# Kernel tuning notes

Measured on AMD Instinct MI355X. Metric: run time of the kernel, lower is better.

Reference implementation:

```python
import jax, jax.numpy as jnp
import numpy as np

L2_REG = 0.25

def setup_inputs() -> dict:
    key = jax.random.key(0)
    k0, k1, k2, k3 = jax.random.split(key, 4)
    B, D, A, K = 16384, 128, 8192, 64
    image_embed = jax.random.normal(k0, (B, D), dtype=jnp.float32)
    anc_ind = jax.random.randint(k1, (A,), 0, B, dtype=jnp.int64)
    pos_ind = jax.random.randint(k2, (A,), 0, B, dtype=jnp.int64)
    neg_ind = jax.random.randint(k3, (A, K), 0, B, dtype=jnp.int64)
    return {"image_embed": image_embed, "anc_ind": anc_ind,
            "pos_ind": pos_ind, "neg_ind": neg_ind}

def reference(image_embed, anc_ind, pos_ind, neg_ind):
    # Gather anchor/positive/negative embeddings
    a = image_embed[anc_ind]          # [A, D]
    p = image_embed[pos_ind]          # [A, D]
    n = image_embed[neg_ind]          # [A, K, D]
    # inner[i, k] = a_i . (n_ik - p_i)
    inner = jnp.einsum('ad,akd->ak', a, n - p[:, None, :])  # [A, K]
    # log(1 + sum_k exp(inner)) computed stably via logaddexp(0, logsumexp)
    per_anchor = jnp.logaddexp(jnp.float32(0.0), jax.nn.logsumexp(inner, axis=1))
    npair = jnp.mean(per_anchor)
    # l2 term: mean L2 norm of all batch embeddings, added once per anchor / len -> once
    l2 = L2_REG * jnp.mean(jnp.linalg.norm(image_embed, axis=1))
    return npair + l2
```

## Files before the change

### kernel.cpp

```cpp
#include <hip/hip_runtime.h>
#include <math.h>

#define B_SZ 16384
#define D_DIM 128
#define A_SZ 8192
#define K_SZ 64
#define L2_REG_F 0.25f
#define NBLK 2048

__device__ __forceinline__ float wave_reduce_sum(float v) {
    #pragma unroll
    for (int off = 32; off > 0; off >>= 1)
        v += __shfl_xor(v, off, 64);
    return v;
}

__device__ __forceinline__ float wave_reduce_max(float v) {
    #pragma unroll
    for (int off = 32; off > 0; off >>= 1)
        v = fmaxf(v, __shfl_xor(v, off, 64));
    return v;
}

__device__ __forceinline__ float dot4(float4 a, float4 b) {
    return a.x * b.x + a.y * b.y + a.z * b.z + a.w * b.w;
}

__global__ __launch_bounds__(256) void fused_kernel(const float* __restrict__ embed,
                                                    const int* __restrict__ anc_ind,
                                                    const int* __restrict__ pos_ind,
                                                    const int* __restrict__ neg_ind,
                                                    float* __restrict__ partial) {
    __shared__ float red[4];
    const int wave = threadIdx.x >> 6;
    const int lane = threadIdx.x & 63;
    const int i    = blockIdx.x * 4 + wave;
    const int g    = lane >> 3;
    const int c    = lane & 7;

    const int4* nb = (const int4*)(neg_ind + (size_t)i * K_SZ + g * 8);
    int4 nlo = nb[0], nhi = nb[1];

    const int ai = anc_ind[i];
    const int pi = pos_ind[i];
    const float4* a4 = (const float4*)(embed + (size_t)ai * D_DIM);
    const float4* p4 = (const float4*)(embed + (size_t)pi * D_DIM);
    float4 A0 = a4[c], A1 = a4[c + 8], A2 = a4[c + 16], A3 = a4[c + 24];
    float4 P0 = p4[c], P1 = p4[c + 8], P2 = p4[c + 16], P3 = p4[c + 24];

    const int r0   = blockIdx.x * 8 + wave * 2;
    const int half = lane >> 5;
    const int hl   = lane & 31;
    float4 nv = ((const float4*)(embed + (size_t)(r0 + half) * D_DIM))[hl];

    int nidx[8] = {nlo.x, nlo.y, nlo.z, nlo.w, nhi.x, nhi.y, nhi.z, nhi.w};
    float s[8];
    #pragma unroll
    for (int p = 0; p < 8; ++p) {
        const float4* nr = (const float4*)(embed + (size_t)nidx[p] * D_DIM);
        float4 n0 = nr[c], n1 = nr[c + 8], n2 = nr[c + 16], n3 = nr[c + 24];
        s[p] = dot4(A0, n0) + dot4(A1, n1) + dot4(A2, n2) + dot4(A3, n3);
    }

    float app = dot4(A0, P0) + dot4(A1, P1) + dot4(A2, P2) + dot4(A3, P3);
    app += __shfl_xor(app, 1, 64);
    app += __shfl_xor(app, 2, 64);
    app += __shfl_xor(app, 4, 64);

    float sq = nv.x * nv.x + nv.y * nv.y + nv.z * nv.z + nv.w * nv.w;
    #pragma unroll
    for (int off = 16; off > 0; off >>= 1)
        sq += __shfl_xor(sq, off, 64);
    float nrm = sqrtf(sq);
    nrm += __shfl_xor(nrm, 32, 64);

    const bool h4 = (c & 4) != 0;
    float t0 = (h4 ? s[4] : s[0]) + __shfl_xor(h4 ? s[0] : s[4], 4, 64);
    float t1 = (h4 ? s[5] : s[1]) + __shfl_xor(h4 ? s[1] : s[5], 4, 64);
    float t2 = (h4 ? s[6] : s[2]) + __shfl_xor(h4 ? s[2] : s[6], 4, 64);
    float t3 = (h4 ? s[7] : s[3]) + __shfl_xor(h4 ? s[3] : s[7], 4, 64);
    const bool h2 = (c & 2) != 0;
    float u0 = (h2 ? t2 : t0) + __shfl_xor(h2 ? t0 : t2, 2, 64);
    float u1 = (h2 ? t3 : t1) + __shfl_xor(h2 ? t1 : t3, 2, 64);
    const bool h1 = (c & 1) != 0;
    float inner = (h1 ? u1 : u0) + __shfl_xor(h1 ? u0 : u1, 1, 64);

    inner -= app;

    float m  = wave_reduce_max(inner);
    float se = wave_reduce_sum(__expf(inner - m));
    float lse = m + __logf(se);
    float per = (lse > 0.f) ? lse + log1pf(__expf(-lse)) : log1pf(__expf(lse));

    if (lane == 0)
        red[wave] = per * (1.0f / (float)A_SZ) + nrm * (L2_REG_F / (float)B_SZ);
    __syncthreads();
    if (threadIdx.x == 0)
        partial[blockIdx.x] = red[0] + red[1] + red[2] + red[3];
}

__global__ __launch_bounds__(256) void finalize_kernel(const float* __restrict__ partial,
                                                       int n, float* __restrict__ out) {
    __shared__ float red[4];
    const int wave = threadIdx.x >> 6;
    const int lane = threadIdx.x & 63;
    float v = 0.f;
    for (int j = threadIdx.x; j < n; j += 256) v += partial[j];
    v = wave_reduce_sum(v);
    if (lane == 0) red[wave] = v;
    __syncthreads();
    if (threadIdx.x == 0)
        out[0] = red[0] + red[1] + red[2] + red[3];
}

extern "C" void kernel_launch(void* const* d_in, const int* in_sizes, int n_in,
                              void* d_out, int out_size, void* d_ws, size_t ws_size,
                              hipStream_t stream) {
    const float* embed = (const float*)d_in[0];
    const int*   anc   = (const int*)d_in[1];
    const int*   pos   = (const int*)d_in[2];
    const int*   neg   = (const int*)d_in[3];
    float* out = (float*)d_out;

    float* partial = (float*)d_ws;
    fused_kernel<<<NBLK, 256, 0, stream>>>(embed, anc, pos, neg, partial);
    finalize_kernel<<<1, 256, 0, stream>>>(partial, NBLK, out);
}
```

Measured before the change: 91.20 us.

## Split each anchor's negatives across two waves and merge logsumexp in shared memory

Each anchor is now handled by two waves of 32 negatives each instead of one wave of 64, so the grid doubles to 4096 blocks and each thread issues 4 row gathers instead of 8. Partial max and sum-exp per wave are merged through shared memory by thread 0 with a rescaled logsumexp. The norm term now uses one row per wave read as float2. The aim is more memory-level parallelism and occupancy from lower register pressure, at the cost of more blocks, duplicated anchor and positive loads, and a serial merge step.

```diff
diff --git a/kernel.cpp b/kernel.cpp
--- a/kernel.cpp
+++ b/kernel.cpp
@@ -6,7 +6,7 @@
 #define A_SZ 8192
 #define K_SZ 64
 #define L2_REG_F 0.25f
-#define NBLK 2048
+#define NBLK 4096
 
 __device__ __forceinline__ float wave_reduce_sum(float v) {
     #pragma unroll
@@ -31,72 +31,74 @@
                                                     const int* __restrict__ pos_ind,
                                                     const int* __restrict__ neg_ind,
                                                     float* __restrict__ partial) {
-    __shared__ float red[4];
+    __shared__ float mw[4], sew[4], nw[4];
     const int wave = threadIdx.x >> 6;
     const int lane = threadIdx.x & 63;
-    const int i    = blockIdx.x * 4 + wave;
+    const int i    = blockIdx.x * 2 + (wave >> 1);
+    const int w    = wave & 1;
     const int g    = lane >> 3;
     const int c    = lane & 7;
 
-    const int4* nb = (const int4*)(neg_ind + (size_t)i * K_SZ + g * 8);
-    int4 nlo = nb[0], nhi = nb[1];
+    const int4 nb = *(const int4*)(neg_ind + (size_t)i * K_SZ + w * 32 + g * 4);
 
     const int ai = anc_ind[i];
     const int pi = pos_ind[i];
     const float4* a4 = (const float4*)(embed + (size_t)ai * D_DIM);
+    float4 A0 = a4[c], A1 = a4[c + 8], A2 = a4[c + 16], A3 = a4[c + 24];
+
+    const float4* r0 = (const float4*)(embed + (size_t)nb.x * D_DIM);
+    const float4* r1 = (const float4*)(embed + (size_t)nb.y * D_DIM);
+    const float4* r2 = (const float4*)(embed + (size_t)nb.z * D_DIM);
+    const float4* r3 = (const float4*)(embed + (size_t)nb.w * D_DIM);
+    float4 q00 = r0[c], q01 = r0[c + 8], q02 = r0[c + 16], q03 = r0[c + 24];
+    float4 q10 = r1[c], q11 = r1[c + 8], q12 = r1[c + 16], q13 = r1[c + 24];
+    float4 q20 = r2[c], q21 = r2[c + 8], q22 = r2[c + 16], q23 = r2[c + 24];
+    float4 q30 = r3[c], q31 = r3[c + 8], q32 = r3[c + 16], q33 = r3[c + 24];
+
     const float4* p4 = (const float4*)(embed + (size_t)pi * D_DIM);
-    float4 A0 = a4[c], A1 = a4[c + 8], A2 = a4[c + 16], A3 = a4[c + 24];
     float4 P0 = p4[c], P1 = p4[c + 8], P2 = p4[c + 16], P3 = p4[c + 24];
-
-    const int r0   = blockIdx.x * 8 + wave * 2;
-    const int half = lane >> 5;
-    const int hl   = lane & 31;
-    float4 nv = ((const float4*)(embed + (size_t)(r0 + half) * D_DIM))[hl];
-
-    int nidx[8] = {nlo.x, nlo.y, nlo.z, nlo.w, nhi.x, nhi.y, nhi.z, nhi.w};
-    float s[8];
-    #pragma unroll
-    for (int p = 0; p < 8; ++p) {
-        const float4* nr = (const float4*)(embed + (size_t)nidx[p] * D_DIM);
-        float4 n0 = nr[c], n1 = nr[c + 8], n2 = nr[c + 16], n3 = nr[c + 24];
-        s[p] = dot4(A0, n0) + dot4(A1, n1) + dot4(A2, n2) + dot4(A3, n3);
-    }
+    const int nrow_id = blockIdx.x * 4 + wave;
+    float2 nv = ((const float2*)(embed + (size_t)nrow_id * D_DIM))[lane];
 
     float app = dot4(A0, P0) + dot4(A1, P1) + dot4(A2, P2) + dot4(A3, P3);
     app += __shfl_xor(app, 1, 64);
     app += __shfl_xor(app, 2, 64);
     app += __shfl_xor(app, 4, 64);
 
-    float sq = nv.x * nv.x + nv.y * nv.y + nv.z * nv.z + nv.w * nv.w;
-    #pragma unroll
-    for (int off = 16; off > 0; off >>= 1)
-        sq += __shfl_xor(sq, off, 64);
-    float nrm = sqrtf(sq);
-    nrm += __shfl_xor(nrm, 32, 64);
+    float sq = wave_reduce_sum(nv.x * nv.x + nv.y * nv.y);
+
+    float s0 = dot4(A0, q00) + dot4(A1, q01) + dot4(A2, q02) + dot4(A3, q03);
+    float s1 = dot4(A0, q10) + dot4(A1, q11) + dot4(A2, q12) + dot4(A3, q13);
+    float s2 = dot4(A0, q20) + dot4(A1, q21) + dot4(A2, q22) + dot4(A3, q23);
+    float s3 = dot4(A0, q30) + dot4(A1, q31) + dot4(A2, q32) + dot4(A3, q33);
 
     const bool h4 = (c & 4) != 0;
-    float t0 = (h4 ? s[4] : s[0]) + __shfl_xor(h4 ? s[0] : s[4], 4, 64);
-    float t1 = (h4 ? s[5] : s[1]) + __shfl_xor(h4 ? s[1] : s[5], 4, 64);
-    float t2 = (h4 ? s[6] : s[2]) + __shfl_xor(h4 ? s[2] : s[6], 4, 64);
-    float t3 = (h4 ? s[7] : s[3]) + __shfl_xor(h4 ? s[3] : s[7], 4, 64);
+    float t0 = (h4 ? s2 : s0) + __shfl_xor(h4 ? s0 : s2, 4, 64);
+    float t1 = (h4 ? s3 : s1) + __shfl_xor(h4 ? s1 : s3, 4, 64);
     const bool h2 = (c & 2) != 0;
-    float u0 = (h2 ? t2 : t0) + __shfl_xor(h2 ? t0 : t2, 2, 64);
-    float u1 = (h2 ? t3 : t1) + __shfl_xor(h2 ? t1 : t3, 2, 64);
-    const bool h1 = (c & 1) != 0;
-    float inner = (h1 ? u1 : u0) + __shfl_xor(h1 ? u0 : u1, 1, 64);
-
-    inner -= app;
+    float u = (h2 ? t1 : t0) + __shfl_xor(h2 ? t0 : t1, 2, 64);
+    u += __shfl_xor(u, 1, 64);
+    float inner = u - app;
 
     float m  = wave_reduce_max(inner);
-    float se = wave_reduce_sum(__expf(inner - m));
-    float lse = m + __logf(se);
-    float per = (lse > 0.f) ? lse + log1pf(__expf(-lse)) : log1pf(__expf(lse));
+    float se = 0.5f * wave_reduce_sum(__expf(inner - m));
 
-    if (lane == 0)
-        red[wave] = per * (1.0f / (float)A_SZ) + nrm * (L2_REG_F / (float)B_SZ);
+    if (lane == 0) { mw[wave] = m; sew[wave] = se; nw[wave] = sqrtf(sq); }
     __syncthreads();
-    if (threadIdx.x == 0)
-        partial[blockIdx.x] = red[0] + red[1] + red[2] + red[3];
+    if (threadIdx.x == 0) {
+        float total = 0.f;
+        #pragma unroll
+        for (int a = 0; a < 2; ++a) {
+            float m0 = mw[2 * a], m1 = mw[2 * a + 1];
+            float mm = fmaxf(m0, m1);
+            float ss = sew[2 * a] * __expf(m0 - mm) + sew[2 * a + 1] * __expf(m1 - mm);
+            float lse = mm + __logf(ss);
+            float per = (lse > 0.f) ? lse + log1pf(__expf(-lse)) : log1pf(__expf(lse));
+            total += per * (1.0f / (float)A_SZ);
+        }
+        total += (nw[0] + nw[1] + nw[2] + nw[3]) * (L2_REG_F / (float)B_SZ);
+        partial[blockIdx.x] = total;
+    }
 }
 
 __global__ __launch_bounds__(256) void finalize_kernel(const float* __restrict__ partial,
```

Measured after the change: 92.27 us. Within noise of the previous version (+1.2%).
